# Kernel tuning notes

Hardware: AMD Instinct MI355X
Metric: run time of the kernel (lower is better)

Reference implementation:

```python
import jax, jax.numpy as jnp
import numpy as np

HIDDEN = 128
VOCAB = 100000
NUM_CLASSES = 5
N_LEAVES = 65536  # complete binary tree -> 2*N_LEAVES-1 = 131071 nodes


def setup_inputs() -> dict:
    key = jax.random.key(0)
    ks = jax.random.split(key, 24)
    H, C = HIDDEN, NUM_CLASSES

    def w(k, o, i):
        return (jax.random.normal(k, (o, i), jnp.float32) / np.sqrt(i)).astype(jnp.float32)

    def b(k, o):
        return jax.random.normal(k, (o,), jnp.float32) * 0.01

    inp = {
        "leaf_tokens": jax.random.randint(ks[0], (N_LEAVES,), 0, VOCAB, dtype=jnp.int64 if jax.config.jax_enable_x64 else jnp.int32).astype(jnp.int32),
        "node_labels": jax.random.randint(ks[1], (2 * N_LEAVES - 1,), 0, NUM_CLASSES).astype(jnp.int32),
        "embed": jax.random.uniform(ks[2], (VOCAB, H), jnp.float32, -0.5 / H, 0.5 / H),
        "W_i_w": w(ks[3], H, H), "W_i_b": b(ks[4], H),
        "W_o_w": w(ks[5], H, H), "W_o_b": b(ks[6], H),
        "W_u_w": w(ks[7], H, H), "W_u_b": b(ks[8], H),
        "U_i_w": w(ks[9], H, 2 * H), "U_i_b": b(ks[10], H),
        "U_o_w": w(ks[11], H, 2 * H), "U_o_b": b(ks[12], H),
        "U_u_w": w(ks[13], H, 2 * H), "U_u_b": b(ks[14], H),
        "F1_w": w(ks[15], H, H), "F1_b": b(ks[16], H),
        "F2_w": w(ks[17], H, H), "F2_b": b(ks[18], H),
        "out_w": w(ks[19], C, H), "out_b": b(ks[20], C),
    }
    return inp


def reference(leaf_tokens, node_labels, embed,
              W_i_w, W_i_b, W_o_w, W_o_b, W_u_w, W_u_b,
              U_i_w, U_i_b, U_o_w, U_o_b, U_u_w, U_u_b,
              F1_w, F1_b, F2_w, F2_b, out_w, out_b):
    def aff(x, wgt, bias):
        return x @ wgt.T + bias

    # ---- leaves: x = embed[token]; c = sigmoid(W_i x) * tanh(W_u x) ----
    x = embed[leaf_tokens]                          # [L, H]
    i = jax.nn.sigmoid(aff(x, W_i_w, W_i_b))
    o = jax.nn.sigmoid(aff(x, W_o_w, W_o_b))
    u = jnp.tanh(aff(x, W_u_w, W_u_b))
    c = i * u
    h = o * jnp.tanh(c)
    outs = [aff(h, out_w, out_b)]                   # dropout is identity at eval

    # ---- internal levels, bottom-up, all same-depth nodes batched ----
    n_levels = int(np.log2(N_LEAVES))
    for _ in range(n_levels):
        hl, hr = h[0::2], h[1::2]                   # [n/2, H] each
        cl, cr = c[0::2], c[1::2]
        xc = jnp.concatenate([hl, hr], axis=1)      # [n/2, 2H]
        i = jax.nn.sigmoid(aff(xc, U_i_w, U_i_b))
        o = jax.nn.sigmoid(aff(xc, U_o_w, U_o_b))
        u = jnp.tanh(aff(xc, U_u_w, U_u_b))
        f1 = jax.nn.sigmoid(aff(hl, F1_w, F1_b))
        f2 = jax.nn.sigmoid(aff(hr, F2_w, F2_b))
        c = i * u + f1 * cl + f2 * cr
        h = o * jnp.tanh(c)
        outs.append(aff(h, out_w, out_b))

    outputs = jnp.concatenate(outs, axis=0)         # [2L-1, num_classes]
    return outputs, node_labels
```

## Files before the change

### kernel.cpp

```cpp
#include <hip/hip_runtime.h>
#include <hip/hip_bf16.h>
#include <cstdint>
#include <cstddef>

#define HDIM 128
#define NLEAVES 65536
#define TOTAL_NODES 131071

using s8v  = __attribute__((ext_vector_type(8))) short;
using f4v  = __attribute__((ext_vector_type(4))) float;

__device__ __forceinline__ short f2bf(float f){
  __hip_bfloat16 b = __float2bfloat16(f);
  return *reinterpret_cast<short*>(&b);
}
__device__ __forceinline__ float sigm(float x){ return 1.0f/(1.0f + __expf(-x)); }
__device__ __forceinline__ float tanh_(float x){
  float a = fabsf(x);
  float t = __expf(-2.0f*a);
  float r = (1.0f - t)/(1.0f + t);
  return copysignf(r, x);
}
__device__ __forceinline__ float bf2f(short s){
  unsigned int u = ((unsigned int)(unsigned short)s) << 16;
  return __uint_as_float(u);
}

__global__ __launch_bounds__(256) void prep_weights(
    const float* __restrict__ Wi, const float* __restrict__ bi,
    const float* __restrict__ Wo, const float* __restrict__ bo,
    const float* __restrict__ Wu, const float* __restrict__ bu,
    const float* __restrict__ Ui, const float* __restrict__ bUi,
    const float* __restrict__ Uo, const float* __restrict__ bUo,
    const float* __restrict__ Uu, const float* __restrict__ bUu,
    const float* __restrict__ F1, const float* __restrict__ bF1,
    const float* __restrict__ F2, const float* __restrict__ bF2,
    short* __restrict__ Wl_lin, short* __restrict__ Wc_lin,
    float* __restrict__ bl, float* __restrict__ bc)
{
  const int gid = blockIdx.x*256 + threadIdx.x;
  if (gid < 640*256){
    const int row = gid >> 8, k = gid & 255;
    const int g = row >> 7, jj = row & 127;
    float v;
    if      (g == 0) v = Ui[jj*256 + k];
    else if (g == 1) v = Uo[jj*256 + k];
    else if (g == 2) v = Uu[jj*256 + k];
    else if (g == 3) v = (k < 128) ? F1[jj*128 + k] : 0.0f;
    else             v = (k >= 128) ? F2[jj*128 + (k-128)] : 0.0f;
    Wc_lin[gid] = f2bf(v);
  }
  if (gid < 384*128){
    const int row = gid >> 7, k = gid & 127;
    const int g = row >> 7, jj = row & 127;
    const float v = (g == 0) ? Wi[jj*128 + k] : (g == 1) ? Wo[jj*128 + k] : Wu[jj*128 + k];
    Wl_lin[gid] = f2bf(v);
  }
  if (gid < 640){
    const int g = gid >> 7, j = gid & 127;
    bc[gid] = (g==0)?bUi[j]:(g==1)?bUo[j]:(g==2)?bUu[j]:(g==3)?bF1[j]:bF2[j];
  }
  if (gid < 384){
    const int g = gid >> 7, j = gid & 127;
    bl[gid] = (g==0)?bi[j]:(g==1)?bo[j]:bu[j];
  }
}

template<int N>
__device__ __forceinline__ void seg_level(
    const int ct, const int r16, const int kg, const int j,
    const float* cin,
    float*       cout,
    short* AL,
    short* hg,
    const s8v (&biou)[3][8], const s8v (&bf)[2][4],
    const float bi_, const float bo_, const float bu_,
    const float bf1_, const float bf2_)
{
  constexpr int PASSES = (N == 64) ? 2 : 1;
  constexpr int NT     = (N >= 32) ? 2 : 1;

  #pragma unroll
  for (int p = 0; p < PASSES; ++p){
    f4v acc[5][NT];
    #pragma unroll
    for (int g = 0; g < 5; ++g)
      #pragma unroll
      for (int mt = 0; mt < NT; ++mt)
        #pragma unroll
        for (int e = 0; e < 4; ++e) acc[g][mt][e] = 0.0f;

    #pragma unroll
    for (int mt = 0; mt < NT; ++mt){
      const int ar = p*32 + mt*16 + r16;
      const short* hp = AL + ar*256;
      const int sw = (ar & 7) << 3;
      s8v av[8];
      #pragma unroll
      for (int kt = 0; kt < 8; ++kt)
        av[kt] = *reinterpret_cast<const s8v*>(hp + ((kg*8 + kt*32) ^ sw));
      #pragma unroll
      for (int kt = 0; kt < 8; ++kt){
        acc[0][mt] = __builtin_amdgcn_mfma_f32_16x16x32_bf16(av[kt], biou[0][kt], acc[0][mt], 0,0,0);
        acc[1][mt] = __builtin_amdgcn_mfma_f32_16x16x32_bf16(av[kt], biou[1][kt], acc[1][mt], 0,0,0);
        acc[2][mt] = __builtin_amdgcn_mfma_f32_16x16x32_bf16(av[kt], biou[2][kt], acc[2][mt], 0,0,0);
      }
      #pragma unroll
      for (int kt = 0; kt < 4; ++kt){
        acc[3][mt] = __builtin_amdgcn_mfma_f32_16x16x32_bf16(av[kt],   bf[0][kt], acc[3][mt], 0,0,0);
        acc[4][mt] = __builtin_amdgcn_mfma_f32_16x16x32_bf16(av[kt+4], bf[1][kt], acc[4][mt], 0,0,0);
      }
    }

    __syncthreads();

    #pragma unroll
    for (int mt = 0; mt < NT; ++mt){
      #pragma unroll
      for (int r = 0; r < 4; ++r){
        const int m = p*32 + mt*16 + kg*4 + r;
        if (m < N){
          const float iv = sigm(acc[0][mt][r] + bi_);
          const float ov = sigm(acc[1][mt][r] + bo_);
          const float uv = tanh_(acc[2][mt][r] + bu_);
          const float f1 = sigm(acc[3][mt][r] + bf1_);
          const float f2 = sigm(acc[4][mt][r] + bf2_);
          const float cl = cin[(2*m    )*HDIM + j];
          const float cr = cin[(2*m + 1)*HDIM + j];
          const float c  = iv*uv + f1*cl + f2*cr;
          const float hv = ov * tanh_(c);
          cout[m*HDIM + j] = c;
          const short hb = f2bf(hv);
          hg[(size_t)m*HDIM + j] = hb;
          const int ar2 = m >> 1;
          const int s   = (m & 1)*HDIM + j;
          AL[ar2*256 + (s ^ ((ar2 & 7) << 3))] = hb;
        }
      }
    }
    __syncthreads();
  }
}

__global__ __launch_bounds__(512) void subtree_kernel(
    const int*   __restrict__ tok,
    const float* __restrict__ embed,
    const short* __restrict__ Wl,
    const short* __restrict__ Wc,
    const float* __restrict__ bl,
    const float* __restrict__ bc,
    short* __restrict__ h_all,
    float* __restrict__ croot1)
{
  __shared__ short AL[64*256];
  __shared__ float cb0[128*HDIM];
  __shared__ float cb1[64*HDIM];

  const int tid  = threadIdx.x;
  const int lane = tid & 63;
  const int ct   = tid >> 6;
  const int r16  = lane & 15;
  const int kg   = lane >> 4;
  const int j    = ct*16 + r16;
  const int bid  = blockIdx.x;

  const float lbi = bl[j], lbo = bl[HDIM + j], lbu = bl[2*HDIM + j];
  const float bi_ = bc[j], bo_ = bc[HDIM + j], bu_ = bc[2*HDIM + j];
  const float bf1_ = bc[3*HDIM + j], bf2_ = bc[4*HDIM + j];

  s8v wl[3][4];
  #pragma unroll
  for (int g = 0; g < 3; ++g){
    const short* bp = Wl + (size_t)(g*128 + j)*128 + kg*8;
    #pragma unroll
    for (int kt = 0; kt < 4; ++kt)
      wl[g][kt] = *reinterpret_cast<const s8v*>(bp + kt*32);
  }

  #pragma unroll
  for (int ii = 0; ii < 4; ++ii){
    const int chunk = ii*512 + tid;
    const int r  = chunk >> 4;
    const int s0 = (chunk & 15)*8;
    const int t  = tok[bid*128 + r];
    const float* ep = embed + (size_t)t*HDIM + s0;
    const float4 v0 = *reinterpret_cast<const float4*>(ep);
    const float4 v1 = *reinterpret_cast<const float4*>(ep + 4);
    s8v v;
    v[0]=f2bf(v0.x); v[1]=f2bf(v0.y); v[2]=f2bf(v0.z); v[3]=f2bf(v0.w);
    v[4]=f2bf(v1.x); v[5]=f2bf(v1.y); v[6]=f2bf(v1.z); v[7]=f2bf(v1.w);
    *reinterpret_cast<s8v*>(AL + r*128 + (s0 ^ ((r & 7) << 3))) = v;
  }
  __syncthreads();

  #pragma unroll
  for (int p = 0; p < 2; ++p){
    f4v acc[3][4];
    #pragma unroll
    for (int g = 0; g < 3; ++g)
      #pragma unroll
      for (int mt = 0; mt < 4; ++mt)
        #pragma unroll
        for (int e = 0; e < 4; ++e) acc[g][mt][e] = 0.0f;

    #pragma unroll
    for (int mt = 0; mt < 4; ++mt){
      const int ar = p*64 + mt*16 + r16;
      const short* hp = AL + ar*128;
      const int sw = (ar & 7) << 3;
      s8v av[4];
      #pragma unroll
      for (int kt = 0; kt < 4; ++kt)
        av[kt] = *reinterpret_cast<const s8v*>(hp + ((kg*8 + kt*32) ^ sw));
      #pragma unroll
      for (int kt = 0; kt < 4; ++kt){
        acc[0][mt] = __builtin_amdgcn_mfma_f32_16x16x32_bf16(av[kt], wl[0][kt], acc[0][mt], 0,0,0);
        acc[1][mt] = __builtin_amdgcn_mfma_f32_16x16x32_bf16(av[kt], wl[1][kt], acc[1][mt], 0,0,0);
        acc[2][mt] = __builtin_amdgcn_mfma_f32_16x16x32_bf16(av[kt], wl[2][kt], acc[2][mt], 0,0,0);
      }
    }
    __syncthreads();
    #pragma unroll
    for (int mt = 0; mt < 4; ++mt){
      #pragma unroll
      for (int r = 0; r < 4; ++r){
        const int m = p*64 + mt*16 + kg*4 + r;
        const float iv = sigm(acc[0][mt][r] + lbi);
        const float ov = sigm(acc[1][mt][r] + lbo);
        const float uv = tanh_(acc[2][mt][r] + lbu);
        const float c  = iv*uv;
        const float hv = ov * tanh_(c);
        cb0[m*HDIM + j] = c;
        const short hb = f2bf(hv);
        h_all[(size_t)(bid*128 + m)*HDIM + j] = hb;
        const int ar2 = m >> 1;
        const int s   = (m & 1)*HDIM + j;
        AL[ar2*256 + (s ^ ((ar2 & 7) << 3))] = hb;
      }
    }
    __syncthreads();
  }

  s8v biou[3][8];
  s8v bf[2][4];
  #pragma unroll
  for (int g = 0; g < 3; ++g){
    const short* bp = Wc + (size_t)(g*128 + j)*256 + kg*8;
    #pragma unroll
    for (int kt = 0; kt < 8; ++kt)
      biou[g][kt] = *reinterpret_cast<const s8v*>(bp + kt*32);
  }
  {
    const short* bp1 = Wc + (size_t)(3*128 + j)*256 + kg*8;
    const short* bp2 = Wc + (size_t)(4*128 + j)*256 + 128 + kg*8;
    #pragma unroll
    for (int kt = 0; kt < 4; ++kt){
      bf[0][kt] = *reinterpret_cast<const s8v*>(bp1 + kt*32);
      bf[1][kt] = *reinterpret_cast<const s8v*>(bp2 + kt*32);
    }
  }

  seg_level<64>(ct,r16,kg,j, cb0, cb1, AL, h_all + (size_t)(65536  + bid*64)*HDIM, biou, bf, bi_,bo_,bu_,bf1_,bf2_);
  seg_level<32>(ct,r16,kg,j, cb1, cb0, AL, h_all + (size_t)(98304  + bid*32)*HDIM, biou, bf, bi_,bo_,bu_,bf1_,bf2_);
  seg_level<16>(ct,r16,kg,j, cb0, cb1, AL, h_all + (size_t)(114688 + bid*16)*HDIM, biou, bf, bi_,bo_,bu_,bf1_,bf2_);
  seg_level<8 >(ct,r16,kg,j, cb1, cb0, AL, h_all + (size_t)(122880 + bid*8 )*HDIM, biou, bf, bi_,bo_,bu_,bf1_,bf2_);
  seg_level<4 >(ct,r16,kg,j, cb0, cb1, AL, h_all + (size_t)(126976 + bid*4 )*HDIM, biou, bf, bi_,bo_,bu_,bf1_,bf2_);
  seg_level<2 >(ct,r16,kg,j, cb1, cb0, AL, h_all + (size_t)(129024 + bid*2 )*HDIM, biou, bf, bi_,bo_,bu_,bf1_,bf2_);
  seg_level<1 >(ct,r16,kg,j, cb0, croot1 + bid*HDIM, AL, h_all + (size_t)(130048 + bid)*HDIM, biou, bf, bi_,bo_,bu_,bf1_,bf2_);
}

__global__ __launch_bounds__(512) void mid_kernel(
    const short* __restrict__ Wc, const float* __restrict__ bc,
    short* __restrict__ h_all,
    const float* __restrict__ croot1,
    float* __restrict__ croot2)
{
  __shared__ short AL[64*256];
  __shared__ float cb0[64*HDIM];
  __shared__ float cb1[32*HDIM];

  const int tid  = threadIdx.x;
  const int lane = tid & 63;
  const int ct   = tid >> 6;
  const int r16  = lane & 15;
  const int kg   = lane >> 4;
  const int j    = ct*16 + r16;
  const int b    = blockIdx.x;

  const float bi_ = bc[j], bo_ = bc[HDIM + j], bu_ = bc[2*HDIM + j];
  const float bf1_ = bc[3*HDIM + j], bf2_ = bc[4*HDIM + j];

  s8v biou[3][8];
  s8v bf[2][4];
  #pragma unroll
  for (int g = 0; g < 3; ++g){
    const short* bp = Wc + (size_t)(g*128 + j)*256 + kg*8;
    #pragma unroll
    for (int kt = 0; kt < 8; ++kt)
      biou[g][kt] = *reinterpret_cast<const s8v*>(bp + kt*32);
  }
  {
    const short* bp1 = Wc + (size_t)(3*128 + j)*256 + kg*8;
    const short* bp2 = Wc + (size_t)(4*128 + j)*256 + 128 + kg*8;
    #pragma unroll
    for (int kt = 0; kt < 4; ++kt){
      bf[0][kt] = *reinterpret_cast<const s8v*>(bp1 + kt*32);
      bf[1][kt] = *reinterpret_cast<const s8v*>(bp2 + kt*32);
    }
  }

  const short* hsrc = h_all + (size_t)(130048 + b*128)*HDIM;
  #pragma unroll
  for (int ii = 0; ii < 4; ++ii){
    const int chunk = ii*512 + tid;
    const int r  = chunk >> 5;
    const int s0 = (chunk & 31)*8;
    const s8v v = *reinterpret_cast<const s8v*>(hsrc + (size_t)(2*r + (s0 >> 7))*HDIM + (s0 & 127));
    *reinterpret_cast<s8v*>(AL + r*256 + (s0 ^ ((r & 7) << 3))) = v;
  }
  __syncthreads();

  seg_level<64>(ct,r16,kg,j, croot1 + (size_t)b*128*HDIM, cb0, AL, h_all + (size_t)(130560 + b*64)*HDIM, biou, bf, bi_,bo_,bu_,bf1_,bf2_);
  seg_level<32>(ct,r16,kg,j, cb0, cb1, AL, h_all + (size_t)(130816 + b*32)*HDIM, biou, bf, bi_,bo_,bu_,bf1_,bf2_);
  seg_level<16>(ct,r16,kg,j, cb1, cb0, AL, h_all + (size_t)(130944 + b*16)*HDIM, biou, bf, bi_,bo_,bu_,bf1_,bf2_);
  seg_level<8 >(ct,r16,kg,j, cb0, cb1, AL, h_all + (size_t)(131008 + b*8 )*HDIM, biou, bf, bi_,bo_,bu_,bf1_,bf2_);
  seg_level<4 >(ct,r16,kg,j, cb1, cb0, AL, h_all + (size_t)(131040 + b*4 )*HDIM, biou, bf, bi_,bo_,bu_,bf1_,bf2_);
  seg_level<2 >(ct,r16,kg,j, cb0, cb1, AL, h_all + (size_t)(131056 + b*2 )*HDIM, biou, bf, bi_,bo_,bu_,bf1_,bf2_);
  seg_level<1 >(ct,r16,kg,j, cb1, croot2 + b*HDIM, AL, h_all + (size_t)(131064 + b)*HDIM, biou, bf, bi_,bo_,bu_,bf1_,bf2_);
}

__global__ __launch_bounds__(512) void top_kernel(
    const short* __restrict__ Wc, const float* __restrict__ bc,
    short* __restrict__ h_all,
    const float* __restrict__ croot2)
{
  __shared__ short AL[16*256];
  __shared__ float cb0[2*HDIM];
  __shared__ float cb1[1*HDIM];

  const int tid  = threadIdx.x;
  const int lane = tid & 63;
  const int ct   = tid >> 6;
  const int r16  = lane & 15;
  const int kg   = lane >> 4;
  const int j    = ct*16 + r16;

  const float bi_ = bc[j], bo_ = bc[HDIM + j], bu_ = bc[2*HDIM + j];
  const float bf1_ = bc[3*HDIM + j], bf2_ = bc[4*HDIM + j];

  s8v biou[3][8];
  s8v bf[2][4];
  #pragma unroll
  for (int g = 0; g < 3; ++g){
    const short* bp = Wc + (size_t)(g*128 + j)*256 + kg*8;
    #pragma unroll
    for (int kt = 0; kt < 8; ++kt)
      biou[g][kt] = *reinterpret_cast<const s8v*>(bp + kt*32);
  }
  {
    const short* bp1 = Wc + (size_t)(3*128 + j)*256 + kg*8;
    const short* bp2 = Wc + (size_t)(4*128 + j)*256 + 128 + kg*8;
    #pragma unroll
    for (int kt = 0; kt < 4; ++kt){
      bf[0][kt] = *reinterpret_cast<const s8v*>(bp1 + kt*32);
      bf[1][kt] = *reinterpret_cast<const s8v*>(bp2 + kt*32);
    }
  }

  for (int i = tid; i < 16*256/8; i += 512){
    s8v z; 
    #pragma unroll
    for (int e = 0; e < 8; ++e) z[e] = 0;
    *reinterpret_cast<s8v*>(AL + i*8) = z;
  }
  __syncthreads();
  if (tid < 64){
    const int r  = tid >> 5;
    const int s0 = (tid & 31)*8;
    const s8v v = *reinterpret_cast<const s8v*>(h_all + (size_t)(131064 + 2*r + (s0 >> 7))*HDIM + (s0 & 127));
    *reinterpret_cast<s8v*>(AL + r*256 + (s0 ^ ((r & 7) << 3))) = v;
  }
  __syncthreads();

  seg_level<2>(ct,r16,kg,j, croot2, cb0, AL, h_all + (size_t)131068*HDIM, biou, bf, bi_,bo_,bu_,bf1_,bf2_);
  seg_level<1>(ct,r16,kg,j, cb0, cb1, AL, h_all + (size_t)131070*HDIM, biou, bf, bi_,bo_,bu_,bf1_,bf2_);
}

__global__ __launch_bounds__(256) void outproj_kernel(
    const short* __restrict__ h_all,
    const int* __restrict__ labels,
    const float* __restrict__ ow, const float* __restrict__ ob,
    float* __restrict__ out)
{
  __shared__ float wsm[5*HDIM];
  __shared__ float bsm[5];
  for (int i = threadIdx.x; i < 5*HDIM; i += 256) wsm[i] = ow[i];
  if (threadIdx.x < 5) bsm[threadIdx.x] = ob[threadIdx.x];
  __syncthreads();
  const int n = blockIdx.x*256 + threadIdx.x;
  if (n >= TOTAL_NODES) return;
  const s8v* hp = reinterpret_cast<const s8v*>(h_all + (size_t)n*HDIM);
  float acc[5] = {0.f,0.f,0.f,0.f,0.f};
  #pragma unroll
  for (int t = 0; t < 16; ++t){
    const s8v v = hp[t];
    #pragma unroll
    for (int e = 0; e < 8; ++e){
      const float hv = bf2f(v[e]);
      const int jj = t*8 + e;
      #pragma unroll
      for (int c5 = 0; c5 < 5; ++c5) acc[c5] += hv * wsm[c5*HDIM + jj];
    }
  }
  #pragma unroll
  for (int c5 = 0; c5 < 5; ++c5) out[(size_t)n*5 + c5] = acc[c5] + bsm[c5];
  out[(size_t)TOTAL_NODES*5 + n] = (float)labels[n];
}

extern "C" void kernel_launch(void* const* d_in, const int* in_sizes, int n_in,
                              void* d_out, int out_size, void* d_ws, size_t ws_size,
                              hipStream_t stream)
{
  (void)in_sizes; (void)n_in; (void)out_size; (void)ws_size;
  const int*   tok    = (const int*)  d_in[0];
  const int*   labels = (const int*)  d_in[1];
  const float* embed  = (const float*)d_in[2];
  const float* Wi  = (const float*)d_in[3];  const float* bi  = (const float*)d_in[4];
  const float* Wo  = (const float*)d_in[5];  const float* bo  = (const float*)d_in[6];
  const float* Wu  = (const float*)d_in[7];  const float* bu  = (const float*)d_in[8];
  const float* Ui  = (const float*)d_in[9];  const float* bUi = (const float*)d_in[10];
  const float* Uo  = (const float*)d_in[11]; const float* bUo = (const float*)d_in[12];
  const float* Uu  = (const float*)d_in[13]; const float* bUu = (const float*)d_in[14];
  const float* F1  = (const float*)d_in[15]; const float* bF1 = (const float*)d_in[16];
  const float* F2  = (const float*)d_in[17]; const float* bF2 = (const float*)d_in[18];
  const float* ow  = (const float*)d_in[19]; const float* ob  = (const float*)d_in[20];
  float* out = (float*)d_out;

  char* ws = (char*)d_ws;
  size_t off = 0;
  auto alloc = [&](size_t bytes) -> void* {
    void* p = ws + off;
    off += (bytes + 255) & ~(size_t)255;
    return p;
  };
  short* h_all  = (short*)alloc((size_t)131072*HDIM*2);
  float* croot1 = (float*)alloc((size_t)512*HDIM*4);
  float* croot2 = (float*)alloc((size_t)4*HDIM*4);
  short* Wl_lin = (short*)alloc((size_t)384*128*2);
  short* Wc_lin = (short*)alloc((size_t)640*256*2);
  float* bl     = (float*)alloc((size_t)384*4);
  float* bc     = (float*)alloc((size_t)640*4);

  prep_weights<<<640, 256, 0, stream>>>(Wi,bi,Wo,bo,Wu,bu,Ui,bUi,Uo,bUo,Uu,bUu,
                                        F1,bF1,F2,bF2, Wl_lin, Wc_lin, bl, bc);

  subtree_kernel<<<512, 512, 0, stream>>>(tok, embed, Wl_lin, Wc_lin, bl, bc, h_all, croot1);
  mid_kernel<<<4, 512, 0, stream>>>(Wc_lin, bc, h_all, croot1, croot2);
  top_kernel<<<1, 512, 0, stream>>>(Wc_lin, bc, h_all, croot2);

  outproj_kernel<<<(TOTAL_NODES + 255)/256, 256, 0, stream>>>(h_all, labels, ow, ob, out);
}
```

Measured before the change: 272.8 us.

## Store MFMA operands in fragment-major LDS layout and pad cell-state buffers

Replaces the XOR-swizzled row-major LDS tile for the hidden-state operand with a fragment-major layout, so each lane reads its 8-element chunk contiguously. Leaf weights are pre-permuted into the same layout by the prep kernel. Cell-state arrays are padded to a stride of 130 to avoid bank conflicts, and launch bounds now request 2 blocks per CU. The scattered per-element writes into the new layout may themselves cause bank conflicts, and the occupancy hint could force register spills given the large register-resident weight arrays. An unused Wc_st buffer is also written.

```diff
diff --git a/kernel.cpp b/kernel.cpp
--- a/kernel.cpp
+++ b/kernel.cpp
@@ -13,6 +13,10 @@
 __device__ __forceinline__ short f2bf(float f){
   __hip_bfloat16 b = __float2bfloat16(f);
   return *reinterpret_cast<short*>(&b);
+}
+__device__ __forceinline__ float bf2f(short s){
+  unsigned int u = ((unsigned int)(unsigned short)s) << 16;
+  return __uint_as_float(u);
 }
 __device__ __forceinline__ float sigm(float x){ return 1.0f/(1.0f + __expf(-x)); }
 __device__ __forceinline__ float tanh_(float x){
@@ -20,10 +24,6 @@
   float t = __expf(-2.0f*a);
   float r = (1.0f - t)/(1.0f + t);
   return copysignf(r, x);
-}
-__device__ __forceinline__ float bf2f(short s){
-  unsigned int u = ((unsigned int)(unsigned short)s) << 16;
-  return __uint_as_float(u);
 }
 
 __global__ __launch_bounds__(256) void prep_weights(
@@ -35,26 +35,33 @@
     const float* __restrict__ Uu, const float* __restrict__ bUu,
     const float* __restrict__ F1, const float* __restrict__ bF1,
     const float* __restrict__ F2, const float* __restrict__ bF2,
-    short* __restrict__ Wl_lin, short* __restrict__ Wc_lin,
+    short* __restrict__ Wc_lin, short* __restrict__ Wc_st,
+    short* __restrict__ Wl_st,
     float* __restrict__ bl, float* __restrict__ bc)
 {
   const int gid = blockIdx.x*256 + threadIdx.x;
   if (gid < 640*256){
     const int row = gid >> 8, k = gid & 255;
     const int g = row >> 7, jj = row & 127;
+    const int ct = jj >> 4, r16 = jj & 15;
+    const int kt = k >> 5, kg = (k >> 3) & 3, e = k & 7;
     float v;
     if      (g == 0) v = Ui[jj*256 + k];
     else if (g == 1) v = Uo[jj*256 + k];
     else if (g == 2) v = Uu[jj*256 + k];
     else if (g == 3) v = (k < 128) ? F1[jj*128 + k] : 0.0f;
     else             v = (k >= 128) ? F2[jj*128 + (k-128)] : 0.0f;
-    Wc_lin[gid] = f2bf(v);
+    const short s = f2bf(v);
+    Wc_lin[gid] = s;
+    Wc_st[ct*20480 + (g*8 + kt)*512 + (kg*16 + r16)*8 + e] = s;
   }
   if (gid < 384*128){
     const int row = gid >> 7, k = gid & 127;
     const int g = row >> 7, jj = row & 127;
+    const int ct = jj >> 4, r16 = jj & 15;
+    const int kt = k >> 5, kg = (k >> 3) & 3, e = k & 7;
     const float v = (g == 0) ? Wi[jj*128 + k] : (g == 1) ? Wo[jj*128 + k] : Wu[jj*128 + k];
-    Wl_lin[gid] = f2bf(v);
+    Wl_st[ct*6144 + (g*4 + kt)*512 + (kg*16 + r16)*8 + e] = f2bf(v);
   }
   if (gid < 640){
     const int g = gid >> 7, j = gid & 127;
@@ -66,19 +73,19 @@
   }
 }
 
-template<int N>
-__device__ __forceinline__ void seg_level(
+template<int N, int CIN, int COUT>
+__device__ __forceinline__ void lstm_level(
     const int ct, const int r16, const int kg, const int j,
-    const float* cin,
-    float*       cout,
-    short* AL,
-    short* hg,
+    const float* cinF,
+    float* coutF, float* __restrict__ coutG,
+    short* AF, short* __restrict__ hg,
     const s8v (&biou)[3][8], const s8v (&bf)[2][4],
     const float bi_, const float bo_, const float bu_,
     const float bf1_, const float bf2_)
 {
   constexpr int PASSES = (N == 64) ? 2 : 1;
   constexpr int NT     = (N >= 32) ? 2 : 1;
+  const int lane = kg*16 + r16;
 
   #pragma unroll
   for (int p = 0; p < PASSES; ++p){
@@ -92,13 +99,11 @@
 
     #pragma unroll
     for (int mt = 0; mt < NT; ++mt){
-      const int ar = p*32 + mt*16 + r16;
-      const short* hp = AL + ar*256;
-      const int sw = (ar & 7) << 3;
       s8v av[8];
+      const short* base = AF + (p*2 + mt)*4096 + lane*8;
       #pragma unroll
       for (int kt = 0; kt < 8; ++kt)
-        av[kt] = *reinterpret_cast<const s8v*>(hp + ((kg*8 + kt*32) ^ sw));
+        av[kt] = *reinterpret_cast<const s8v*>(base + kt*512);
       #pragma unroll
       for (int kt = 0; kt < 8; ++kt){
         acc[0][mt] = __builtin_amdgcn_mfma_f32_16x16x32_bf16(av[kt], biou[0][kt], acc[0][mt], 0,0,0);
@@ -125,16 +130,23 @@
           const float uv = tanh_(acc[2][mt][r] + bu_);
           const float f1 = sigm(acc[3][mt][r] + bf1_);
           const float f2 = sigm(acc[4][mt][r] + bf2_);
-          const float cl = cin[(2*m    )*HDIM + j];
-          const float cr = cin[(2*m + 1)*HDIM + j];
+          float cl, cr;
+          if constexpr (CIN == 0){
+            cl = cinF[(2*m)*130 + j];   cr = cinF[(2*m+1)*130 + j];
+          } else {
+            cl = cinF[(2*m)*128 + j];   cr = cinF[(2*m+1)*128 + j];
+          }
           const float c  = iv*uv + f1*cl + f2*cr;
           const float hv = ov * tanh_(c);
-          cout[m*HDIM + j] = c;
+          if constexpr (COUT == 0) coutF[m*130 + j] = c;
+          else                     coutG[m*128 + j] = c;
           const short hb = f2bf(hv);
           hg[(size_t)m*HDIM + j] = hb;
-          const int ar2 = m >> 1;
-          const int s   = (m & 1)*HDIM + j;
-          AL[ar2*256 + (s ^ ((ar2 & 7) << 3))] = hb;
+          const int rowp = m >> 1;
+          const int kp   = ((m & 1) << 7) | j;
+          const int ktp  = kp >> 5;
+          const int kgp  = (kp >> 3) & 3;
+          AF[(rowp >> 4)*4096 + ktp*512 + ((kgp << 4) | (rowp & 15))*8 + (kp & 7)] = hb;
         }
       }
     }
@@ -142,19 +154,38 @@
   }
 }
 
-__global__ __launch_bounds__(512) void subtree_kernel(
+__device__ __forceinline__ void load_reg_weights(
+    const short* __restrict__ Wc, const int j, const int kg,
+    s8v (&biou)[3][8], s8v (&bf)[2][4])
+{
+  #pragma unroll
+  for (int g = 0; g < 3; ++g){
+    const short* bp = Wc + (size_t)(g*128 + j)*256 + kg*8;
+    #pragma unroll
+    for (int kt = 0; kt < 8; ++kt)
+      biou[g][kt] = *reinterpret_cast<const s8v*>(bp + kt*32);
+  }
+  const short* bp1 = Wc + (size_t)(3*128 + j)*256 + kg*8;
+  const short* bp2 = Wc + (size_t)(4*128 + j)*256 + 128 + kg*8;
+  #pragma unroll
+  for (int kt = 0; kt < 4; ++kt){
+    bf[0][kt] = *reinterpret_cast<const s8v*>(bp1 + kt*32);
+    bf[1][kt] = *reinterpret_cast<const s8v*>(bp2 + kt*32);
+  }
+}
+
+__global__ __launch_bounds__(512, 2) void subtree_kernel(
     const int*   __restrict__ tok,
     const float* __restrict__ embed,
-    const short* __restrict__ Wl,
-    const short* __restrict__ Wc,
-    const float* __restrict__ bl,
-    const float* __restrict__ bc,
+    const short* __restrict__ Wl_st,
+    const short* __restrict__ Wc_lin,
+    const float* __restrict__ bl, const float* __restrict__ bc,
     short* __restrict__ h_all,
     float* __restrict__ croot1)
 {
-  __shared__ short AL[64*256];
-  __shared__ float cb0[128*HDIM];
-  __shared__ float cb1[64*HDIM];
+  __shared__ short AF[16384];
+  __shared__ float cp0[128*130];
+  __shared__ float cp1[64*130];
 
   const int tid  = threadIdx.x;
   const int lane = tid & 63;
@@ -164,32 +195,28 @@
   const int j    = ct*16 + r16;
   const int bid  = blockIdx.x;
 
+  s8v wl[3][4];
+  #pragma unroll
+  for (int g = 0; g < 3; ++g)
+    #pragma unroll
+    for (int kt = 0; kt < 4; ++kt)
+      wl[g][kt] = *reinterpret_cast<const s8v*>(&Wl_st[ct*6144 + (g*4 + kt)*512 + lane*8]);
   const float lbi = bl[j], lbo = bl[HDIM + j], lbu = bl[2*HDIM + j];
-  const float bi_ = bc[j], bo_ = bc[HDIM + j], bu_ = bc[2*HDIM + j];
-  const float bf1_ = bc[3*HDIM + j], bf2_ = bc[4*HDIM + j];
-
-  s8v wl[3][4];
-  #pragma unroll
-  for (int g = 0; g < 3; ++g){
-    const short* bp = Wl + (size_t)(g*128 + j)*128 + kg*8;
-    #pragma unroll
-    for (int kt = 0; kt < 4; ++kt)
-      wl[g][kt] = *reinterpret_cast<const s8v*>(bp + kt*32);
-  }
-
-  #pragma unroll
-  for (int ii = 0; ii < 4; ++ii){
-    const int chunk = ii*512 + tid;
-    const int r  = chunk >> 4;
-    const int s0 = (chunk & 15)*8;
-    const int t  = tok[bid*128 + r];
-    const float* ep = embed + (size_t)t*HDIM + s0;
+
+  #pragma unroll
+  for (int it = 0; it < 4; ++it){
+    const int cch = it*512 + tid;
+    const int mt = cch >> 8, rem = cch & 255;
+    const int kt = rem >> 6, l2 = rem & 63, kg2 = l2 >> 4, r2 = l2 & 15;
+    const int row = mt*16 + r2;
+    const int t = tok[bid*128 + row];
+    const float* ep = embed + (size_t)t*HDIM + kt*32 + kg2*8;
     const float4 v0 = *reinterpret_cast<const float4*>(ep);
     const float4 v1 = *reinterpret_cast<const float4*>(ep + 4);
     s8v v;
     v[0]=f2bf(v0.x); v[1]=f2bf(v0.y); v[2]=f2bf(v0.z); v[3]=f2bf(v0.w);
     v[4]=f2bf(v1.x); v[5]=f2bf(v1.y); v[6]=f2bf(v1.z); v[7]=f2bf(v1.w);
-    *reinterpret_cast<s8v*>(AL + r*128 + (s0 ^ ((r & 7) << 3))) = v;
+    *reinterpret_cast<s8v*>(AF + mt*2048 + kt*512 + l2*8) = v;
   }
   __syncthreads();
 
@@ -205,13 +232,11 @@
 
     #pragma unroll
     for (int mt = 0; mt < 4; ++mt){
-      const int ar = p*64 + mt*16 + r16;
-      const short* hp = AL + ar*128;
-      const int sw = (ar & 7) << 3;
       s8v av[4];
+      const short* base = AF + (p*4 + mt)*2048 + lane*8;
       #pragma unroll
       for (int kt = 0; kt < 4; ++kt)
-        av[kt] = *reinterpret_cast<const s8v*>(hp + ((kg*8 + kt*32) ^ sw));
+        av[kt] = *reinterpret_cast<const s8v*>(base + kt*512);
       #pragma unroll
       for (int kt = 0; kt < 4; ++kt){
         acc[0][mt] = __builtin_amdgcn_mfma_f32_16x16x32_bf16(av[kt], wl[0][kt], acc[0][mt], 0,0,0);
@@ -230,54 +255,42 @@
         const float uv = tanh_(acc[2][mt][r] + lbu);
         const float c  = iv*uv;
         const float hv = ov * tanh_(c);
-        cb0[m*HDIM + j] = c;
+        cp0[m*130 + j] = c;
         const short hb = f2bf(hv);
         h_all[(size_t)(bid*128 + m)*HDIM + j] = hb;
-        const int ar2 = m >> 1;
-        const int s   = (m & 1)*HDIM + j;
-        AL[ar2*256 + (s ^ ((ar2 & 7) << 3))] = hb;
+        const int rowp = m >> 1;
+        const int kp   = ((m & 1) << 7) | j;
+        const int ktp  = kp >> 5;
+        const int kgp  = (kp >> 3) & 3;
+        AF[(rowp >> 4)*4096 + ktp*512 + ((kgp << 4) | (rowp & 15))*8 + (kp & 7)] = hb;
       }
     }
     __syncthreads();
   }
 
-  s8v biou[3][8];
-  s8v bf[2][4];
-  #pragma unroll
-  for (int g = 0; g < 3; ++g){
-    const short* bp = Wc + (size_t)(g*128 + j)*256 + kg*8;
-    #pragma unroll
-    for (int kt = 0; kt < 8; ++kt)
-      biou[g][kt] = *reinterpret_cast<const s8v*>(bp + kt*32);
-  }
-  {
-    const short* bp1 = Wc + (size_t)(3*128 + j)*256 + kg*8;
-    const short* bp2 = Wc + (size_t)(4*128 + j)*256 + 128 + kg*8;
-    #pragma unroll
-    for (int kt = 0; kt < 4; ++kt){
-      bf[0][kt] = *reinterpret_cast<const s8v*>(bp1 + kt*32);
-      bf[1][kt] = *reinterpret_cast<const s8v*>(bp2 + kt*32);
-    }
-  }
-
-  seg_level<64>(ct,r16,kg,j, cb0, cb1, AL, h_all + (size_t)(65536  + bid*64)*HDIM, biou, bf, bi_,bo_,bu_,bf1_,bf2_);
-  seg_level<32>(ct,r16,kg,j, cb1, cb0, AL, h_all + (size_t)(98304  + bid*32)*HDIM, biou, bf, bi_,bo_,bu_,bf1_,bf2_);
-  seg_level<16>(ct,r16,kg,j, cb0, cb1, AL, h_all + (size_t)(114688 + bid*16)*HDIM, biou, bf, bi_,bo_,bu_,bf1_,bf2_);
-  seg_level<8 >(ct,r16,kg,j, cb1, cb0, AL, h_all + (size_t)(122880 + bid*8 )*HDIM, biou, bf, bi_,bo_,bu_,bf1_,bf2_);
-  seg_level<4 >(ct,r16,kg,j, cb0, cb1, AL, h_all + (size_t)(126976 + bid*4 )*HDIM, biou, bf, bi_,bo_,bu_,bf1_,bf2_);
-  seg_level<2 >(ct,r16,kg,j, cb1, cb0, AL, h_all + (size_t)(129024 + bid*2 )*HDIM, biou, bf, bi_,bo_,bu_,bf1_,bf2_);
-  seg_level<1 >(ct,r16,kg,j, cb0, croot1 + bid*HDIM, AL, h_all + (size_t)(130048 + bid)*HDIM, biou, bf, bi_,bo_,bu_,bf1_,bf2_);
-}
-
-__global__ __launch_bounds__(512) void mid_kernel(
+  s8v biou[3][8]; s8v bf[2][4];
+  load_reg_weights(Wc_lin, j, kg, biou, bf);
+  const float bi_ = bc[j], bo_ = bc[HDIM + j], bu_ = bc[2*HDIM + j];
+  const float bf1_ = bc[3*HDIM + j], bf2_ = bc[4*HDIM + j];
+
+  lstm_level<64,0,0>(ct,r16,kg,j, cp0, cp1, nullptr, AF, h_all + (size_t)(65536  + bid*64)*HDIM, biou, bf, bi_,bo_,bu_,bf1_,bf2_);
+  lstm_level<32,0,0>(ct,r16,kg,j, cp1, cp0, nullptr, AF, h_all + (size_t)(98304  + bid*32)*HDIM, biou, bf, bi_,bo_,bu_,bf1_,bf2_);
+  lstm_level<16,0,0>(ct,r16,kg,j, cp0, cp1, nullptr, AF, h_all + (size_t)(114688 + bid*16)*HDIM, biou, bf, bi_,bo_,bu_,bf1_,bf2_);
+  lstm_level<8 ,0,0>(ct,r16,kg,j, cp1, cp0, nullptr, AF, h_all + (size_t)(122880 + bid*8 )*HDIM, biou, bf, bi_,bo_,bu_,bf1_,bf2_);
+  lstm_level<4 ,0,0>(ct,r16,kg,j, cp0, cp1, nullptr, AF, h_all + (size_t)(126976 + bid*4 )*HDIM, biou, bf, bi_,bo_,bu_,bf1_,bf2_);
+  lstm_level<2 ,0,0>(ct,r16,kg,j, cp1, cp0, nullptr, AF, h_all + (size_t)(129024 + bid*2 )*HDIM, biou, bf, bi_,bo_,bu_,bf1_,bf2_);
+  lstm_level<1 ,0,1>(ct,r16,kg,j, cp0, nullptr, croot1 + (size_t)bid*HDIM, AF, h_all + (size_t)(130048 + bid)*HDIM, biou, bf, bi_,bo_,bu_,bf1_,bf2_);
+}
+
+__global__ __launch_bounds__(512, 2) void mid_kernel(
     const short* __restrict__ Wc, const float* __restrict__ bc,
     short* __restrict__ h_all,
     const float* __restrict__ croot1,
     float* __restrict__ croot2)
 {
-  __shared__ short AL[64*256];
-  __shared__ float cb0[64*HDIM];
-  __shared__ float cb1[32*HDIM];
+  __shared__ short AF[16384];
+  __shared__ float cp0[64*130];
+  __shared__ float cp1[32*130];
 
   const int tid  = threadIdx.x;
   const int lane = tid & 63;
@@ -287,56 +300,40 @@
   const int j    = ct*16 + r16;
   const int b    = blockIdx.x;
 
+  s8v biou[3][8]; s8v bf[2][4];
+  load_reg_weights(Wc, j, kg, biou, bf);
   const float bi_ = bc[j], bo_ = bc[HDIM + j], bu_ = bc[2*HDIM + j];
   const float bf1_ = bc[3*HDIM + j], bf2_ = bc[4*HDIM + j];
 
-  s8v biou[3][8];
-  s8v bf[2][4];
-  #pragma unroll
-  for (int g = 0; g < 3; ++g){
-    const short* bp = Wc + (size_t)(g*128 + j)*256 + kg*8;
-    #pragma unroll
-    for (int kt = 0; kt < 8; ++kt)
-      biou[g][kt] = *reinterpret_cast<const s8v*>(bp + kt*32);
-  }
-  {
-    const short* bp1 = Wc + (size_t)(3*128 + j)*256 + kg*8;
-    const short* bp2 = Wc + (size_t)(4*128 + j)*256 + 128 + kg*8;
-    #pragma unroll
-    for (int kt = 0; kt < 4; ++kt){
-      bf[0][kt] = *reinterpret_cast<const s8v*>(bp1 + kt*32);
-      bf[1][kt] = *reinterpret_cast<const s8v*>(bp2 + kt*32);
-    }
-  }
-
-  const short* hsrc = h_all + (size_t)(130048 + b*128)*HDIM;
-  #pragma unroll
-  for (int ii = 0; ii < 4; ++ii){
-    const int chunk = ii*512 + tid;
-    const int r  = chunk >> 5;
-    const int s0 = (chunk & 31)*8;
-    const s8v v = *reinterpret_cast<const s8v*>(hsrc + (size_t)(2*r + (s0 >> 7))*HDIM + (s0 & 127));
-    *reinterpret_cast<s8v*>(AL + r*256 + (s0 ^ ((r & 7) << 3))) = v;
+  const short* h7 = h_all + (size_t)(130048 + b*128)*HDIM;
+  #pragma unroll
+  for (int it = 0; it < 4; ++it){
+    const int cch = it*512 + tid;
+    const int mt = cch >> 9, rem = cch & 511;
+    const int kt = rem >> 6, l2 = rem & 63, kg2 = l2 >> 4, r2 = l2 & 15;
+    const int rowp = mt*16 + r2;
+    const short* src = h7 + (size_t)(2*rowp + (kt>>2))*HDIM + (kt&3)*32 + kg2*8;
+    *reinterpret_cast<s8v*>(AF + cch*8) = *reinterpret_cast<const s8v*>(src);
   }
   __syncthreads();
 
-  seg_level<64>(ct,r16,kg,j, croot1 + (size_t)b*128*HDIM, cb0, AL, h_all + (size_t)(130560 + b*64)*HDIM, biou, bf, bi_,bo_,bu_,bf1_,bf2_);
-  seg_level<32>(ct,r16,kg,j, cb0, cb1, AL, h_all + (size_t)(130816 + b*32)*HDIM, biou, bf, bi_,bo_,bu_,bf1_,bf2_);
-  seg_level<16>(ct,r16,kg,j, cb1, cb0, AL, h_all + (size_t)(130944 + b*16)*HDIM, biou, bf, bi_,bo_,bu_,bf1_,bf2_);
-  seg_level<8 >(ct,r16,kg,j, cb0, cb1, AL, h_all + (size_t)(131008 + b*8 )*HDIM, biou, bf, bi_,bo_,bu_,bf1_,bf2_);
-  seg_level<4 >(ct,r16,kg,j, cb1, cb0, AL, h_all + (size_t)(131040 + b*4 )*HDIM, biou, bf, bi_,bo_,bu_,bf1_,bf2_);
-  seg_level<2 >(ct,r16,kg,j, cb0, cb1, AL, h_all + (size_t)(131056 + b*2 )*HDIM, biou, bf, bi_,bo_,bu_,bf1_,bf2_);
-  seg_level<1 >(ct,r16,kg,j, cb1, croot2 + b*HDIM, AL, h_all + (size_t)(131064 + b)*HDIM, biou, bf, bi_,bo_,bu_,bf1_,bf2_);
-}
-
-__global__ __launch_bounds__(512) void top_kernel(
+  lstm_level<64,2,0>(ct,r16,kg,j, croot1 + (size_t)b*128*HDIM, cp0, nullptr, AF, h_all + (size_t)(130560 + b*64)*HDIM, biou, bf, bi_,bo_,bu_,bf1_,bf2_);
+  lstm_level<32,0,0>(ct,r16,kg,j, cp0, cp1, nullptr, AF, h_all + (size_t)(130816 + b*32)*HDIM, biou, bf, bi_,bo_,bu_,bf1_,bf2_);
+  lstm_level<16,0,0>(ct,r16,kg,j, cp1, cp0, nullptr, AF, h_all + (size_t)(130944 + b*16)*HDIM, biou, bf, bi_,bo_,bu_,bf1_,bf2_);
+  lstm_level<8 ,0,0>(ct,r16,kg,j, cp0, cp1, nullptr, AF, h_all + (size_t)(131008 + b*8 )*HDIM, biou, bf, bi_,bo_,bu_,bf1_,bf2_);
+  lstm_level<4 ,0,0>(ct,r16,kg,j, cp1, cp0, nullptr, AF, h_all + (size_t)(131040 + b*4 )*HDIM, biou, bf, bi_,bo_,bu_,bf1_,bf2_);
+  lstm_level<2 ,0,0>(ct,r16,kg,j, cp0, cp1, nullptr, AF, h_all + (size_t)(131056 + b*2 )*HDIM, biou, bf, bi_,bo_,bu_,bf1_,bf2_);
+  lstm_level<1 ,0,1>(ct,r16,kg,j, cp1, nullptr, croot2 + (size_t)b*HDIM, AF, h_all + (size_t)(131064 + b)*HDIM, biou, bf, bi_,bo_,bu_,bf1_,bf2_);
+}
+
+__global__ __launch_bounds__(512, 2) void top_kernel(
     const short* __restrict__ Wc, const float* __restrict__ bc,
     short* __restrict__ h_all,
     const float* __restrict__ croot2)
 {
-  __shared__ short AL[16*256];
-  __shared__ float cb0[2*HDIM];
-  __shared__ float cb1[1*HDIM];
+  __shared__ short AF[4096];
+  __shared__ float cp0[2*130];
+  __shared__ float cp1[1*130];
 
   const int tid  = threadIdx.x;
   const int lane = tid & 63;
@@ -345,45 +342,23 @@
   const int kg   = lane >> 4;
   const int j    = ct*16 + r16;
 
+  s8v biou[3][8]; s8v bf[2][4];
+  load_reg_weights(Wc, j, kg, biou, bf);
   const float bi_ = bc[j], bo_ = bc[HDIM + j], bu_ = bc[2*HDIM + j];
   const float bf1_ = bc[3*HDIM + j], bf2_ = bc[4*HDIM + j];
 
-  s8v biou[3][8];
-  s8v bf[2][4];
-  #pragma unroll
-  for (int g = 0; g < 3; ++g){
-    const short* bp = Wc + (size_t)(g*128 + j)*256 + kg*8;
-    #pragma unroll
-    for (int kt = 0; kt < 8; ++kt)
-      biou[g][kt] = *reinterpret_cast<const s8v*>(bp + kt*32);
-  }
-  {
-    const short* bp1 = Wc + (size_t)(3*128 + j)*256 + kg*8;
-    const short* bp2 = Wc + (size_t)(4*128 + j)*256 + 128 + kg*8;
-    #pragma unroll
-    for (int kt = 0; kt < 4; ++kt){
-      bf[0][kt] = *reinterpret_cast<const s8v*>(bp1 + kt*32);
-      bf[1][kt] = *reinterpret_cast<const s8v*>(bp2 + kt*32);
-    }
-  }
-
-  for (int i = tid; i < 16*256/8; i += 512){
-    s8v z; 
-    #pragma unroll
-    for (int e = 0; e < 8; ++e) z[e] = 0;
-    *reinterpret_cast<s8v*>(AL + i*8) = z;
+  if (tid < 512){
+    const int cch = tid;
+    const int kt = cch >> 6, l2 = cch & 63, kg2 = l2 >> 4, r2 = l2 & 15;
+    int hrow = 2*r2 + (kt >> 2);
+    if (hrow > 7) hrow = 7;
+    const short* src = h_all + (size_t)(131064 + hrow)*HDIM + (kt&3)*32 + kg2*8;
+    *reinterpret_cast<s8v*>(AF + kt*512 + l2*8) = *reinterpret_cast<const s8v*>(src);
   }
   __syncthreads();
-  if (tid < 64){
-    const int r  = tid >> 5;
-    const int s0 = (tid & 31)*8;
-    const s8v v = *reinterpret_cast<const s8v*>(h_all + (size_t)(131064 + 2*r + (s0 >> 7))*HDIM + (s0 & 127));
-    *reinterpret_cast<s8v*>(AL + r*256 + (s0 ^ ((r & 7) << 3))) = v;
-  }
-  __syncthreads();
-
-  seg_level<2>(ct,r16,kg,j, croot2, cb0, AL, h_all + (size_t)131068*HDIM, biou, bf, bi_,bo_,bu_,bf1_,bf2_);
-  seg_level<1>(ct,r16,kg,j, cb0, cb1, AL, h_all + (size_t)131070*HDIM, biou, bf, bi_,bo_,bu_,bf1_,bf2_);
+
+  lstm_level<2,2,0>(ct,r16,kg,j, croot2, cp0, nullptr, AF, h_all + (size_t)131068*HDIM, biou, bf, bi_,bo_,bu_,bf1_,bf2_);
+  lstm_level<1,0,0>(ct,r16,kg,j, cp0, cp1, nullptr, AF, h_all + (size_t)131070*HDIM, biou, bf, bi_,bo_,bu_,bf1_,bf2_);
 }
 
 __global__ __launch_bounds__(256) void outproj_kernel(
@@ -446,15 +421,16 @@
   short* h_all  = (short*)alloc((size_t)131072*HDIM*2);
   float* croot1 = (float*)alloc((size_t)512*HDIM*4);
   float* croot2 = (float*)alloc((size_t)4*HDIM*4);
-  short* Wl_lin = (short*)alloc((size_t)384*128*2);
   short* Wc_lin = (short*)alloc((size_t)640*256*2);
+  short* Wc_st  = (short*)alloc((size_t)640*256*2);
+  short* Wl_st  = (short*)alloc((size_t)384*128*2);
   float* bl     = (float*)alloc((size_t)384*4);
   float* bc     = (float*)alloc((size_t)640*4);
 
   prep_weights<<<640, 256, 0, stream>>>(Wi,bi,Wo,bo,Wu,bu,Ui,bUi,Uo,bUo,Uu,bUu,
-                                        F1,bF1,F2,bF2, Wl_lin, Wc_lin, bl, bc);
-
-  subtree_kernel<<<512, 512, 0, stream>>>(tok, embed, Wl_lin, Wc_lin, bl, bc, h_all, croot1);
+                                        F1,bF1,F2,bF2, Wc_lin, Wc_st, Wl_st, bl, bc);
+
+  subtree_kernel<<<512, 512, 0, stream>>>(tok, embed, Wl_st, Wc_lin, bl, bc, h_all, croot1);
   mid_kernel<<<4, 512, 0, stream>>>(Wc_lin, bc, h_all, croot1, croot2);
   top_kernel<<<1, 512, 0, stream>>>(Wc_lin, bc, h_all, croot2);
 
```

New measurement: 267.6 us. Within noise of the previous version (-1.9%).
